# Performance work log

Measured on AMD Instinct MI355X. Metric: run time of the kernel, lower is better.

## Reference

```python
import jax, jax.numpy as jnp
import numpy as np

N_EMBD = 1024
EXPAND = 2
D_INNER = N_EMBD * EXPAND          # 2048
D_STATE = 64
N_HEADS = D_INNER // D_STATE       # 32
HEAD_DIM = D_INNER // N_HEADS      # 64
N_GROUPS = 1
D_CONV = 4
N_LAYERS = 48
BATCH, SEQ = 1, 512
PROJ_SIZE = 2 * D_INNER + N_HEADS + 2 * N_GROUPS * D_STATE  # 4256
EPS = 1e-6


def setup_inputs() -> dict:
    key = jax.random.key(0)
    ks = jax.random.split(key, 6)
    init_std = 0.02
    proj_std = 0.02 / np.sqrt(2 * N_LAYERS)
    return {
        "x": jax.random.normal(ks[0], (BATCH, SEQ, N_EMBD), jnp.float32),
        "norm_scale": jnp.ones((N_EMBD,), jnp.float32),
        "w_in": jax.random.normal(ks[1], (N_EMBD, PROJ_SIZE), jnp.float32) * init_std,
        "conv_weight": jax.random.normal(ks[2], (D_CONV, D_INNER), jnp.float32) * 0.02,
        "conv_bias": jnp.zeros((D_INNER,), jnp.float32),
        "A_log": jnp.log(0.5 + jnp.arange(N_HEADS, dtype=jnp.float32) * 0.5 / N_HEADS),
        "dt_bias": jax.random.normal(ks[3], (N_HEADS,), jnp.float32) * 0.1,
        "w_out": jax.random.normal(ks[4], (D_INNER, N_EMBD), jnp.float32) * proj_std,
    }


def _mamba_fwd(x, norm_scale, w_in, conv_weight, conv_bias, A_log, dt_bias, w_out):
    b, T, _ = x.shape
    residual = x
    # RMSNorm
    xn = x * jax.lax.rsqrt(jnp.mean(x * x, axis=-1, keepdims=True) + EPS) * norm_scale
    # in_proj and split
    proj = xn @ w_in  # (b, T, proj_size)
    gate = proj[..., :D_INNER]
    ssm_in = proj[..., D_INNER:2 * D_INNER]
    dt_raw = proj[..., 2 * D_INNER:2 * D_INNER + N_HEADS]
    gs = N_GROUPS * D_STATE
    B = proj[..., 2 * D_INNER + N_HEADS:2 * D_INNER + N_HEADS + gs].reshape(b, T, N_GROUPS, D_STATE)
    C = proj[..., 2 * D_INNER + N_HEADS + gs:].reshape(b, T, N_GROUPS, D_STATE)
    # causal depthwise short conv (cross-correlation, matching lax.conv semantics)
    xp = jnp.pad(ssm_in, ((0, 0), (D_CONV - 1, 0), (0, 0)))
    conv = conv_bias + sum(conv_weight[k] * xp[:, k:k + T, :] for k in range(D_CONV))
    h = jax.nn.silu(conv)  # (b, T, d_inner)
    dt = jax.nn.softplus(dt_raw + dt_bias)  # (b, T, H)
    A = -jnp.exp(A_log)  # (H,)
    A_bar = jnp.exp(A[None, None, :] * dt)  # (b, T, H)
    # heads / groups
    hpg = N_HEADS // N_GROUPS
    xh = h.reshape(b, T, N_HEADS, HEAD_DIM)
    Bh = jnp.repeat(B, hpg, axis=2)  # (b, T, H, N)
    Ch = jnp.repeat(C, hpg, axis=2)  # (b, T, H, N)
    # Bu[b,t,h,p,n] = B[b,t,h,n] * dt[b,t,h] * x[b,t,h,p]
    Bu = Bh[:, :, :, None, :] * (dt[..., None, None] * xh[..., None])  # (b,T,H,P,N)

    def _binary_op(left, right):
        a_l, b_l = left
        a_r, b_r = right
        return (a_l * a_r, a_r * b_l + b_r)

    # A_bar broadcast to (b,T,H,1,1) so the pair broadcasts against Bu
    _, states = jax.lax.associative_scan(_binary_op, (A_bar[..., None, None], Bu), axis=1)
    y = jnp.einsum('bthpn,bthn->bthp', states, Ch).reshape(b, T, D_INNER)
    y = y * jax.nn.silu(gate)
    y = y @ w_out
    return residual + y


def reference(x, norm_scale, w_in, conv_weight, conv_bias, A_log, dt_bias, w_out):
    return _mamba_fwd(x, norm_scale, w_in, conv_weight, conv_bias, A_log, dt_bias, w_out)
```

## Files before the change

kernel.cpp:

```cpp
#include <hip/hip_runtime.h>
#include <hip/hip_bf16.h>

typedef unsigned short u16;
typedef float f32x4v __attribute__((ext_vector_type(4)));
typedef short short8 __attribute__((ext_vector_type(8)));

#define TSEQ 512
#define EMB  1024
#define DI   2048
#define NH   32
#define DS   64
#define PROJ 4256
#define PROJP 4352
#define NCH  8
#define LCH  64
#define KSPLIT2 4

__device__ __forceinline__ u16 f2bf(float f) {
    union { __hip_bfloat16 h; u16 u; } cv;
    cv.h = __float2bfloat16(f);
    return cv.u;
}
__device__ __forceinline__ unsigned pack2(float a, float b) {
    return (unsigned)f2bf(a) | ((unsigned)f2bf(b) << 16);
}
__device__ __forceinline__ float silu(float v) { return v / (1.f + expf(-v)); }

__device__ __forceinline__ void transpose_tile(
        const float* __restrict__ src, u16* __restrict__ dst,
        int K, int N, int n0, int k0, int tid, float tile[64][68]) {
    const int lr = tid >> 4;
    const int lc = tid & 15;
    #pragma unroll
    for (int ps = 0; ps < 4; ++ps) {
        int r = ps * 16 + lr;
        float4 v;
        if (n0 + lc * 4 + 3 < N) {
            v = *(const float4*)&src[(size_t)(k0 + r) * N + n0 + lc * 4];
        } else {
            float t0 = 0.f, t1 = 0.f, t2 = 0.f, t3 = 0.f;
            int nb = n0 + lc * 4;
            if (nb + 0 < N) t0 = src[(size_t)(k0 + r) * N + nb + 0];
            if (nb + 1 < N) t1 = src[(size_t)(k0 + r) * N + nb + 1];
            if (nb + 2 < N) t2 = src[(size_t)(k0 + r) * N + nb + 2];
            if (nb + 3 < N) t3 = src[(size_t)(k0 + r) * N + nb + 3];
            v = make_float4(t0, t1, t2, t3);
        }
        *(float4*)&tile[r][lc * 4] = v;
    }
    __syncthreads();
    const int kk2 = (tid & 31) * 2;
    const int nr  = tid >> 5;
    #pragma unroll
    for (int ps = 0; ps < 8; ++ps) {
        int n = ps * 8 + nr;
        unsigned o = (unsigned)f2bf(tile[kk2][n]) | ((unsigned)f2bf(tile[kk2 + 1][n]) << 16);
        *(unsigned*)&dst[(size_t)(n0 + n) * K + k0 + kk2] = o;
    }
}

__global__ __launch_bounds__(256) void k_prep(
        const float* __restrict__ w_in, u16* __restrict__ w_inT,
        const float* __restrict__ w_out, u16* __restrict__ w_outT,
        const float* __restrict__ x, const float* __restrict__ scale,
        u16* __restrict__ xnb) {
    __shared__ float tile[64][68];
    const int b = blockIdx.x;
    const int tid = threadIdx.x;
    if (b < 1088) {
        int bx = b % 68, by = b / 68;
        transpose_tile(w_in, w_inT, 1024, PROJ, bx * 64, by * 64, tid, tile);
    } else if (b < 1600) {
        int b2 = b - 1088;
        int bx = b2 % 16, by = b2 / 16;
        transpose_tile(w_out, w_outT, 2048, 1024, bx * 64, by * 64, tid, tile);
    } else {
        int t = b - 1600;
        const float4* xr = (const float4*)(x + (size_t)t * EMB);
        float4 v = xr[tid];
        float ss = v.x * v.x + v.y * v.y + v.z * v.z + v.w * v.w;
        #pragma unroll
        for (int off = 32; off; off >>= 1) ss += __shfl_xor(ss, off);
        if ((tid & 63) == 0) tile[0][tid >> 6] = ss;
        __syncthreads();
        float tot = tile[0][0] + tile[0][1] + tile[0][2] + tile[0][3];
        float inv = rsqrtf(tot * (1.f / EMB) + 1e-6f);
        float4 s = ((const float4*)scale)[tid];
        uint2 o;
        o.x = pack2(v.x * inv * s.x, v.y * inv * s.y);
        o.y = pack2(v.z * inv * s.z, v.w * inv * s.w);
        ((uint2*)xnb)[(size_t)t * 256 + tid] = o;
    }
}

template<int BM, int BN>
__global__ __launch_bounds__(256) void k_gemm(
        const u16* __restrict__ A, int lda,
        const u16* __restrict__ BT, int ldb,
        float* __restrict__ C, int ldc, int Kper) {
    constexpr int WM = BM / 2, WN = BN / 2, FM = WM / 16, FN = WN / 16;
    constexpr int NA = BM * 8 / 256, NB = BN * 8 / 256;
    __shared__ __align__(16) u16 Al[BM][72];
    __shared__ __align__(16) u16 Bl[BN][72];
    const int tid = threadIdx.x;
    const int wid = tid >> 6, lane = tid & 63;
    const int wr = wid >> 1, wc = wid & 1;
    const int ar = lane & 15, kg = lane >> 4;
    const int row0 = blockIdx.y * BM, col0 = blockIdx.x * BN;
    const int kbase = blockIdx.z * Kper;
    const int Mtot = gridDim.y * BM;
    float* Cz = C + (size_t)blockIdx.z * Mtot * ldc;

    short8 ra[NA], rb[NB];
    auto load_stage = [&](int k0) {
        #pragma unroll
        for (int j = 0; j < NA; ++j) {
            int idx = tid + j * 256;
            ra[j] = *(const short8*)(A + (size_t)(row0 + (idx >> 3)) * lda + k0 + (idx & 7) * 8);
        }
        #pragma unroll
        for (int j = 0; j < NB; ++j) {
            int idx = tid + j * 256;
            rb[j] = *(const short8*)(BT + (size_t)(col0 + (idx >> 3)) * ldb + k0 + (idx & 7) * 8);
        }
    };
    auto write_stage = [&]() {
        #pragma unroll
        for (int j = 0; j < NA; ++j) {
            int idx = tid + j * 256;
            *(short8*)&Al[idx >> 3][(idx & 7) * 8] = ra[j];
        }
        #pragma unroll
        for (int j = 0; j < NB; ++j) {
            int idx = tid + j * 256;
            *(short8*)&Bl[idx >> 3][(idx & 7) * 8] = rb[j];
        }
    };

    f32x4v acc[FM][FN] = {};
    const int NT = Kper / 64;
    load_stage(kbase);
    for (int kt = 0; kt < NT; ++kt) {
        write_stage();
        __syncthreads();
        if (kt + 1 < NT) load_stage(kbase + (kt + 1) * 64);
        #pragma unroll
        for (int kk = 0; kk < 2; ++kk) {
            short8 af[FM], bf[FN];
            #pragma unroll
            for (int m = 0; m < FM; ++m)
                af[m] = *(const short8*)&Al[wr * WM + m * 16 + ar][kk * 32 + kg * 8];
            #pragma unroll
            for (int n = 0; n < FN; ++n)
                bf[n] = *(const short8*)&Bl[wc * WN + n * 16 + ar][kk * 32 + kg * 8];
            #pragma unroll
            for (int m = 0; m < FM; ++m)
                #pragma unroll
                for (int n = 0; n < FN; ++n)
                    acc[m][n] = __builtin_amdgcn_mfma_f32_16x16x32_bf16(
                        af[m], bf[n], acc[m][n], 0, 0, 0);
        }
        __syncthreads();
    }
    #pragma unroll
    for (int m = 0; m < FM; ++m)
        #pragma unroll
        for (int n = 0; n < FN; ++n)
            #pragma unroll
            for (int j = 0; j < 4; ++j) {
                int row = row0 + wr * WM + m * 16 + kg * 4 + j;
                int col = col0 + wc * WN + n * 16 + ar;
                Cz[(size_t)row * ldc + col] = acc[m][n][j];
            }
}

__global__ __launch_bounds__(256) void k_reduce_out(
        const float* __restrict__ part, const float* __restrict__ x,
        float* __restrict__ out) {
    int i = blockIdx.x * 256 + threadIdx.x;
    float4 v = ((const float4*)x)[i];
    #pragma unroll
    for (int z = 0; z < KSPLIT2; ++z) {
        float4 p = ((const float4*)part)[(size_t)z * (TSEQ * EMB / 4) + i];
        v.x += p.x; v.y += p.y; v.z += p.z; v.w += p.w;
    }
    ((float4*)out)[i] = v;
}

__global__ __launch_bounds__(256) void k_scan1f(
        const float* __restrict__ proj, const float* __restrict__ cw,
        const float* __restrict__ cb, const float* __restrict__ A_log,
        const float* __restrict__ dt_bias,
        float* __restrict__ Sloc, float* __restrict__ Pc) {
    const int c = blockIdx.x, h = blockIdx.y;
    const int tid = threadIdx.x;
    const int q = tid & 3, p = tid >> 2, n0 = q * 16;
    __shared__ __align__(16) float Blds[64][64];
    __shared__ __align__(16) float xt[67][64];
    __shared__ float al[64], dl[64];
    for (int i = tid; i < 4096; i += 256) {
        int t = i >> 6, n = i & 63;
        Blds[t][n] = proj[(size_t)(c * 64 + t) * PROJP + 2 * DI + NH + n];
    }
    for (int i = tid; i < 67 * 64; i += 256) {
        int r = i >> 6, n = i & 63;
        int tt = c * 64 - 3 + r;
        xt[r][n] = (tt >= 0) ? proj[(size_t)tt * PROJP + DI + h * 64 + n] : 0.f;
    }
    if (tid < 64) {
        float z = proj[(size_t)(c * 64 + tid) * PROJP + 2 * DI + h] + dt_bias[h];
        float dt = (z > 20.f) ? z : log1pf(expf(z));
        dl[tid] = dt;
        al[tid] = expf(-expf(A_log[h]) * dt);
    }
    __syncthreads();
    const int ch = h * 64 + p;
    const float cw0 = cw[0 * DI + ch], cw1 = cw[1 * DI + ch];
    const float cw2 = cw[2 * DI + ch], cw3 = cw[3 * DI + ch];
    const float cbv = cb[ch];
    float x0 = xt[0][p], x1 = xt[1][p], x2 = xt[2][p];
    float s[16] = {};
    for (int t = 0; t < 64; ++t) {
        float x3 = xt[t + 3][p];
        float cv = cbv + cw0 * x0 + cw1 * x1 + cw2 * x2 + cw3 * x3;
        x0 = x1; x1 = x2; x2 = x3;
        float hv = silu(cv);
        float a = al[t];
        float dtx = dl[t] * hv;
        const float4* brow = (const float4*)&Blds[t][n0];
        #pragma unroll
        for (int i4 = 0; i4 < 4; ++i4) {
            float4 b = brow[i4];
            s[i4*4+0] = a * s[i4*4+0] + dtx * b.x;
            s[i4*4+1] = a * s[i4*4+1] + dtx * b.y;
            s[i4*4+2] = a * s[i4*4+2] + dtx * b.z;
            s[i4*4+3] = a * s[i4*4+3] + dtx * b.w;
        }
    }
    float* dst = Sloc + ((size_t)(c * 32 + h) * 64 + p) * 64 + n0;
    #pragma unroll
    for (int i4 = 0; i4 < 4; ++i4)
        ((float4*)dst)[i4] = make_float4(s[i4*4], s[i4*4+1], s[i4*4+2], s[i4*4+3]);
    if (tid == 0) {
        float pr = 1.f;
        for (int t = 0; t < 64; ++t) pr *= al[t];
        Pc[c * 32 + h] = pr;
    }
}

__global__ __launch_bounds__(256) void k_scan3f(
        const float* __restrict__ proj, const float* __restrict__ cw,
        const float* __restrict__ cb, const float* __restrict__ A_log,
        const float* __restrict__ dt_bias,
        const float* __restrict__ Sloc, const float* __restrict__ Pc,
        u16* __restrict__ yg) {
    const int c = blockIdx.x, h = blockIdx.y;
    const int tid = threadIdx.x;
    const int q = tid & 3, p = tid >> 2, n0 = q * 16;
    __shared__ __align__(16) float Blds[64][64];
    __shared__ __align__(16) float Clds[64][64];
    __shared__ __align__(16) float xt[67][64];
    __shared__ float al[64], dl[64];
    for (int i = tid; i < 4096; i += 256) {
        int t = i >> 6, n = i & 63;
        Blds[t][n] = proj[(size_t)(c * 64 + t) * PROJP + 2 * DI + NH + n];
        Clds[t][n] = proj[(size_t)(c * 64 + t) * PROJP + 2 * DI + NH + DS + n];
    }
    for (int i = tid; i < 67 * 64; i += 256) {
        int r = i >> 6, n = i & 63;
        int tt = c * 64 - 3 + r;
        xt[r][n] = (tt >= 0) ? proj[(size_t)tt * PROJP + DI + h * 64 + n] : 0.f;
    }
    if (tid < 64) {
        float z = proj[(size_t)(c * 64 + tid) * PROJP + 2 * DI + h] + dt_bias[h];
        float dt = (z > 20.f) ? z : log1pf(expf(z));
        dl[tid] = dt;
        al[tid] = expf(-expf(A_log[h]) * dt);
    }
    __syncthreads();
    float s[16] = {};
    for (int j = 0; j < c; ++j) {
        float pcv = Pc[j * 32 + h];
        const float4* sj = (const float4*)(Sloc + ((size_t)(j * 32 + h) * 64 + p) * 64 + n0);
        #pragma unroll
        for (int i4 = 0; i4 < 4; ++i4) {
            float4 v = sj[i4];
            s[i4*4+0] = pcv * s[i4*4+0] + v.x;
            s[i4*4+1] = pcv * s[i4*4+1] + v.y;
            s[i4*4+2] = pcv * s[i4*4+2] + v.z;
            s[i4*4+3] = pcv * s[i4*4+3] + v.w;
        }
    }
    const int ch = h * 64 + p;
    const float cw0 = cw[0 * DI + ch], cw1 = cw[1 * DI + ch];
    const float cw2 = cw[2 * DI + ch], cw3 = cw[3 * DI + ch];
    const float cbv = cb[ch];
    float x0 = xt[0][p], x1 = xt[1][p], x2 = xt[2][p];
    for (int t = 0; t < 64; ++t) {
        float x3 = xt[t + 3][p];
        float cv = cbv + cw0 * x0 + cw1 * x1 + cw2 * x2 + cw3 * x3;
        x0 = x1; x1 = x2; x2 = x3;
        float hv = silu(cv);
        float a = al[t];
        float dtx = dl[t] * hv;
        const float4* brow = (const float4*)&Blds[t][n0];
        const float4* crow = (const float4*)&Clds[t][n0];
        float yp = 0.f;
        #pragma unroll
        for (int i4 = 0; i4 < 4; ++i4) {
            float4 b = brow[i4], cc = crow[i4];
            s[i4*4+0] = a * s[i4*4+0] + dtx * b.x; yp += s[i4*4+0] * cc.x;
            s[i4*4+1] = a * s[i4*4+1] + dtx * b.y; yp += s[i4*4+1] * cc.y;
            s[i4*4+2] = a * s[i4*4+2] + dtx * b.z; yp += s[i4*4+2] * cc.z;
            s[i4*4+3] = a * s[i4*4+3] + dtx * b.w; yp += s[i4*4+3] * cc.w;
        }
        yp += __shfl_xor(yp, 1);
        yp += __shfl_xor(yp, 2);
        if (q == 0) xt[t][p] = yp;
    }
    __syncthreads();
    for (int i = tid; i < 4096; i += 256) {
        int t = i >> 6, pp = i & 63;
        float y = xt[t][pp];
        float g = proj[(size_t)(c * 64 + t) * PROJP + h * 64 + pp];
        yg[(size_t)(c * 64 + t) * DI + h * 64 + pp] = f2bf(y * silu(g));
    }
}

extern "C" void kernel_launch(void* const* d_in, const int* in_sizes, int n_in,
                              void* d_out, int out_size, void* d_ws, size_t ws_size,
                              hipStream_t stream) {
    (void)in_sizes; (void)n_in; (void)out_size; (void)ws_size;
    const float* x       = (const float*)d_in[0];
    const float* nscale  = (const float*)d_in[1];
    const float* w_in    = (const float*)d_in[2];
    const float* conv_w  = (const float*)d_in[3];
    const float* conv_b  = (const float*)d_in[4];
    const float* A_log   = (const float*)d_in[5];
    const float* dt_bias = (const float*)d_in[6];
    const float* w_out   = (const float*)d_in[7];
    float* out = (float*)d_out;

    char* wsp = (char*)d_ws;
    auto alloc = [&](size_t bytes) {
        char* ptr = wsp;
        wsp += (bytes + 255) & ~(size_t)255;
        return ptr;
    };
    u16*   w_inT  = (u16*)  alloc((size_t)PROJP * 1024 * 2);
    u16*   w_outT = (u16*)  alloc((size_t)1024 * 2048 * 2);
    u16*   xnb    = (u16*)  alloc((size_t)512 * 1024 * 2);
    float* proj   = (float*)alloc((size_t)512 * PROJP * 4);
    float* Pc     = (float*)alloc((size_t)256 * 4);
    float* Sloc   = (float*)alloc((size_t)NCH * 32 * 4096 * 4);
    u16*   yg     = (u16*)  alloc((size_t)512 * 2048 * 2);
    float* part2  = (float*)alloc((size_t)KSPLIT2 * 512 * 1024 * 4);

    k_prep<<<2112, 256, 0, stream>>>(w_in, w_inT, w_out, w_outT, x, nscale, xnb);
    k_gemm<32, 128><<<dim3(34, 16, 1), 256, 0, stream>>>(
        xnb, 1024, w_inT, 1024, proj, PROJP, 1024);
    k_scan1f<<<dim3(NCH, 32), 256, 0, stream>>>(
        proj, conv_w, conv_b, A_log, dt_bias, Sloc, Pc);
    k_scan3f<<<dim3(NCH, 32), 256, 0, stream>>>(
        proj, conv_w, conv_b, A_log, dt_bias, Sloc, Pc, yg);
    k_gemm<32, 128><<<dim3(8, 16, KSPLIT2), 256, 0, stream>>>(
        yg, 2048, w_outT, 2048, part2, 1024, 2048 / KSPLIT2);
    k_reduce_out<<<512, 256, 0, stream>>>(part2, x, out);
}
```

Baseline: 171.6 us.

## Restructure chunked scan into local pass, inter-chunk state pass, and correction

The two-kernel chunked scan, which recomputed the local recurrence in the second pass, becomes three stages. First, a local intra-chunk scan emits per-chunk states, cumulative decay products and local outputs. Second, a small kernel propagates initial states across chunks. Third, a correction kernel adds the C·S_init·Pcum contribution and applies the gate. Chunk count doubles to 16 with 32 steps each, which raises parallelism and removes the serial recurrence recompute. The cost is extra global traffic for yloc and Sinit and one more launch.

```diff
diff --git a/kernel.cpp b/kernel.cpp
--- a/kernel.cpp
+++ b/kernel.cpp
@@ -12,8 +12,8 @@
 #define DS   64
 #define PROJ 4256
 #define PROJP 4352
-#define NCH  8
-#define LCH  64
+#define NCH  16
+#define LCH  32
 #define KSPLIT2 4
 
 __device__ __forceinline__ u16 f2bf(float f) {
@@ -187,116 +187,50 @@
     ((float4*)out)[i] = v;
 }
 
-__global__ __launch_bounds__(256) void k_scan1f(
+__global__ __launch_bounds__(256) void k_scan1g(
         const float* __restrict__ proj, const float* __restrict__ cw,
         const float* __restrict__ cb, const float* __restrict__ A_log,
         const float* __restrict__ dt_bias,
-        float* __restrict__ Sloc, float* __restrict__ Pc) {
+        float* __restrict__ Sloc, float* __restrict__ Pcum,
+        float* __restrict__ yloc) {
     const int c = blockIdx.x, h = blockIdx.y;
     const int tid = threadIdx.x;
     const int q = tid & 3, p = tid >> 2, n0 = q * 16;
-    __shared__ __align__(16) float Blds[64][64];
-    __shared__ __align__(16) float xt[67][64];
-    __shared__ float al[64], dl[64];
-    for (int i = tid; i < 4096; i += 256) {
+    __shared__ __align__(16) float Blds[LCH][64];
+    __shared__ __align__(16) float Clds[LCH][64];
+    __shared__ __align__(16) float xt[LCH + 3][64];
+    __shared__ float al[LCH], dl[LCH];
+    __shared__ float yl[LCH][64];
+    for (int i = tid; i < LCH * 64; i += 256) {
         int t = i >> 6, n = i & 63;
-        Blds[t][n] = proj[(size_t)(c * 64 + t) * PROJP + 2 * DI + NH + n];
-    }
-    for (int i = tid; i < 67 * 64; i += 256) {
+        Blds[t][n] = proj[(size_t)(c * LCH + t) * PROJP + 2 * DI + NH + n];
+        Clds[t][n] = proj[(size_t)(c * LCH + t) * PROJP + 2 * DI + NH + DS + n];
+    }
+    for (int i = tid; i < (LCH + 3) * 64; i += 256) {
         int r = i >> 6, n = i & 63;
-        int tt = c * 64 - 3 + r;
+        int tt = c * LCH - 3 + r;
         xt[r][n] = (tt >= 0) ? proj[(size_t)tt * PROJP + DI + h * 64 + n] : 0.f;
     }
-    if (tid < 64) {
-        float z = proj[(size_t)(c * 64 + tid) * PROJP + 2 * DI + h] + dt_bias[h];
+    if (tid < LCH) {
+        float z = proj[(size_t)(c * LCH + tid) * PROJP + 2 * DI + h] + dt_bias[h];
         float dt = (z > 20.f) ? z : log1pf(expf(z));
         dl[tid] = dt;
         al[tid] = expf(-expf(A_log[h]) * dt);
     }
     __syncthreads();
+    if (tid < LCH) {
+        float pr = 1.f;
+        #pragma unroll
+        for (int k = 0; k < LCH; ++k) if (k <= tid) pr *= al[k];
+        Pcum[((size_t)(c * 32 + h)) * LCH + tid] = pr;
+    }
     const int ch = h * 64 + p;
     const float cw0 = cw[0 * DI + ch], cw1 = cw[1 * DI + ch];
     const float cw2 = cw[2 * DI + ch], cw3 = cw[3 * DI + ch];
     const float cbv = cb[ch];
     float x0 = xt[0][p], x1 = xt[1][p], x2 = xt[2][p];
     float s[16] = {};
-    for (int t = 0; t < 64; ++t) {
-        float x3 = xt[t + 3][p];
-        float cv = cbv + cw0 * x0 + cw1 * x1 + cw2 * x2 + cw3 * x3;
-        x0 = x1; x1 = x2; x2 = x3;
-        float hv = silu(cv);
-        float a = al[t];
-        float dtx = dl[t] * hv;
-        const float4* brow = (const float4*)&Blds[t][n0];
-        #pragma unroll
-        for (int i4 = 0; i4 < 4; ++i4) {
-            float4 b = brow[i4];
-            s[i4*4+0] = a * s[i4*4+0] + dtx * b.x;
-            s[i4*4+1] = a * s[i4*4+1] + dtx * b.y;
-            s[i4*4+2] = a * s[i4*4+2] + dtx * b.z;
-            s[i4*4+3] = a * s[i4*4+3] + dtx * b.w;
-        }
-    }
-    float* dst = Sloc + ((size_t)(c * 32 + h) * 64 + p) * 64 + n0;
-    #pragma unroll
-    for (int i4 = 0; i4 < 4; ++i4)
-        ((float4*)dst)[i4] = make_float4(s[i4*4], s[i4*4+1], s[i4*4+2], s[i4*4+3]);
-    if (tid == 0) {
-        float pr = 1.f;
-        for (int t = 0; t < 64; ++t) pr *= al[t];
-        Pc[c * 32 + h] = pr;
-    }
-}
-
-__global__ __launch_bounds__(256) void k_scan3f(
-        const float* __restrict__ proj, const float* __restrict__ cw,
-        const float* __restrict__ cb, const float* __restrict__ A_log,
-        const float* __restrict__ dt_bias,
-        const float* __restrict__ Sloc, const float* __restrict__ Pc,
-        u16* __restrict__ yg) {
-    const int c = blockIdx.x, h = blockIdx.y;
-    const int tid = threadIdx.x;
-    const int q = tid & 3, p = tid >> 2, n0 = q * 16;
-    __shared__ __align__(16) float Blds[64][64];
-    __shared__ __align__(16) float Clds[64][64];
-    __shared__ __align__(16) float xt[67][64];
-    __shared__ float al[64], dl[64];
-    for (int i = tid; i < 4096; i += 256) {
-        int t = i >> 6, n = i & 63;
-        Blds[t][n] = proj[(size_t)(c * 64 + t) * PROJP + 2 * DI + NH + n];
-        Clds[t][n] = proj[(size_t)(c * 64 + t) * PROJP + 2 * DI + NH + DS + n];
-    }
-    for (int i = tid; i < 67 * 64; i += 256) {
-        int r = i >> 6, n = i & 63;
-        int tt = c * 64 - 3 + r;
-        xt[r][n] = (tt >= 0) ? proj[(size_t)tt * PROJP + DI + h * 64 + n] : 0.f;
-    }
-    if (tid < 64) {
-        float z = proj[(size_t)(c * 64 + tid) * PROJP + 2 * DI + h] + dt_bias[h];
-        float dt = (z > 20.f) ? z : log1pf(expf(z));
-        dl[tid] = dt;
-        al[tid] = expf(-expf(A_log[h]) * dt);
-    }
-    __syncthreads();
-    float s[16] = {};
-    for (int j = 0; j < c; ++j) {
-        float pcv = Pc[j * 32 + h];
-        const float4* sj = (const float4*)(Sloc + ((size_t)(j * 32 + h) * 64 + p) * 64 + n0);
-        #pragma unroll
-        for (int i4 = 0; i4 < 4; ++i4) {
-            float4 v = sj[i4];
-            s[i4*4+0] = pcv * s[i4*4+0] + v.x;
-            s[i4*4+1] = pcv * s[i4*4+1] + v.y;
-            s[i4*4+2] = pcv * s[i4*4+2] + v.z;
-            s[i4*4+3] = pcv * s[i4*4+3] + v.w;
-        }
-    }
-    const int ch = h * 64 + p;
-    const float cw0 = cw[0 * DI + ch], cw1 = cw[1 * DI + ch];
-    const float cw2 = cw[2 * DI + ch], cw3 = cw[3 * DI + ch];
-    const float cbv = cb[ch];
-    float x0 = xt[0][p], x1 = xt[1][p], x2 = xt[2][p];
-    for (int t = 0; t < 64; ++t) {
+    for (int t = 0; t < LCH; ++t) {
         float x3 = xt[t + 3][p];
         float cv = cbv + cw0 * x0 + cw1 * x1 + cw2 * x2 + cw3 * x3;
         x0 = x1; x1 = x2; x2 = x3;
@@ -316,14 +250,78 @@
         }
         yp += __shfl_xor(yp, 1);
         yp += __shfl_xor(yp, 2);
-        if (q == 0) xt[t][p] = yp;
-    }
-    __syncthreads();
+        if (q == 0) yl[t][p] = yp;
+    }
+    float* dst = Sloc + ((size_t)(c * 32 + h) * 64 + p) * 64 + n0;
+    #pragma unroll
+    for (int i4 = 0; i4 < 4; ++i4)
+        ((float4*)dst)[i4] = make_float4(s[i4*4], s[i4*4+1], s[i4*4+2], s[i4*4+3]);
+    __syncthreads();
+    for (int i = tid; i < LCH * 64; i += 256) {
+        int t = i >> 6, pp = i & 63;
+        yloc[(size_t)(c * LCH + t) * DI + h * 64 + pp] = yl[t][pp];
+    }
+}
+
+__global__ __launch_bounds__(256) void k_scan2(
+        const float* __restrict__ Sloc, const float* __restrict__ Pcum,
+        float* __restrict__ Sinit) {
+    int gid = blockIdx.x * 256 + threadIdx.x;
+    int h = gid >> 12, rem = gid & 4095;
+    float s = 0.f;
+    #pragma unroll
+    for (int cc = 0; cc < NCH; ++cc) {
+        size_t o = (size_t)(cc * 32 + h) * 4096 + rem;
+        Sinit[o] = s;
+        s = Pcum[((size_t)(cc * 32 + h)) * LCH + (LCH - 1)] * s + Sloc[o];
+    }
+}
+
+__global__ __launch_bounds__(256) void k_corr(
+        const float* __restrict__ proj, const float* __restrict__ Sinit,
+        const float* __restrict__ Pcum, const float* __restrict__ yloc,
+        u16* __restrict__ yg) {
+    const int c = blockIdx.x, h = blockIdx.y;
+    const int tid = threadIdx.x;
+    const int q = tid & 3, p = tid >> 2, n0 = q * 16;
+    __shared__ __align__(16) float Clds[LCH][64];
+    __shared__ __align__(16) float Sl[64][68];
+    __shared__ float Pl[LCH];
+    __shared__ float yl[LCH][64];
+    for (int i = tid; i < LCH * 64; i += 256) {
+        int t = i >> 6, n = i & 63;
+        Clds[t][n] = proj[(size_t)(c * LCH + t) * PROJP + 2 * DI + NH + DS + n];
+    }
     for (int i = tid; i < 4096; i += 256) {
+        Sl[i >> 6][i & 63] = Sinit[(size_t)(c * 32 + h) * 4096 + i];
+    }
+    if (tid < LCH) Pl[tid] = Pcum[((size_t)(c * 32 + h)) * LCH + tid];
+    __syncthreads();
+    float st[16];
+    #pragma unroll
+    for (int i4 = 0; i4 < 4; ++i4) {
+        float4 v = *(const float4*)&Sl[p][n0 + i4 * 4];
+        st[i4*4+0] = v.x; st[i4*4+1] = v.y; st[i4*4+2] = v.z; st[i4*4+3] = v.w;
+    }
+    for (int t = 0; t < LCH; ++t) {
+        const float4* crow = (const float4*)&Clds[t][n0];
+        float acc = 0.f;
+        #pragma unroll
+        for (int i4 = 0; i4 < 4; ++i4) {
+            float4 cc4 = crow[i4];
+            acc += st[i4*4+0] * cc4.x + st[i4*4+1] * cc4.y
+                 + st[i4*4+2] * cc4.z + st[i4*4+3] * cc4.w;
+        }
+        acc += __shfl_xor(acc, 1);
+        acc += __shfl_xor(acc, 2);
+        if (q == 0) yl[t][p] = acc * Pl[t];
+    }
+    __syncthreads();
+    for (int i = tid; i < LCH * 64; i += 256) {
         int t = i >> 6, pp = i & 63;
-        float y = xt[t][pp];
-        float g = proj[(size_t)(c * 64 + t) * PROJP + h * 64 + pp];
-        yg[(size_t)(c * 64 + t) * DI + h * 64 + pp] = f2bf(y * silu(g));
+        float y = yloc[(size_t)(c * LCH + t) * DI + h * 64 + pp] + yl[t][pp];
+        float g = proj[(size_t)(c * LCH + t) * PROJP + h * 64 + pp];
+        yg[(size_t)(c * LCH + t) * DI + h * 64 + pp] = f2bf(y * silu(g));
     }
 }
 
@@ -351,18 +349,20 @@
     u16*   w_outT = (u16*)  alloc((size_t)1024 * 2048 * 2);
     u16*   xnb    = (u16*)  alloc((size_t)512 * 1024 * 2);
     float* proj   = (float*)alloc((size_t)512 * PROJP * 4);
-    float* Pc     = (float*)alloc((size_t)256 * 4);
+    float* Pcum   = (float*)alloc((size_t)NCH * 32 * LCH * 4);
     float* Sloc   = (float*)alloc((size_t)NCH * 32 * 4096 * 4);
+    float* Sinit  = (float*)alloc((size_t)NCH * 32 * 4096 * 4);
+    float* yloc   = (float*)alloc((size_t)512 * 2048 * 4);
     u16*   yg     = (u16*)  alloc((size_t)512 * 2048 * 2);
     float* part2  = (float*)alloc((size_t)KSPLIT2 * 512 * 1024 * 4);
 
     k_prep<<<2112, 256, 0, stream>>>(w_in, w_inT, w_out, w_outT, x, nscale, xnb);
     k_gemm<32, 128><<<dim3(34, 16, 1), 256, 0, stream>>>(
         xnb, 1024, w_inT, 1024, proj, PROJP, 1024);
-    k_scan1f<<<dim3(NCH, 32), 256, 0, stream>>>(
-        proj, conv_w, conv_b, A_log, dt_bias, Sloc, Pc);
-    k_scan3f<<<dim3(NCH, 32), 256, 0, stream>>>(
-        proj, conv_w, conv_b, A_log, dt_bias, Sloc, Pc, yg);
+    k_scan1g<<<dim3(NCH, 32), 256, 0, stream>>>(
+        proj, conv_w, conv_b, A_log, dt_bias, Sloc, Pcum, yloc);
+    k_scan2<<<512, 256, 0, stream>>>(Sloc, Pcum, Sinit);
+    k_corr<<<dim3(NCH, 32), 256, 0, stream>>>(proj, Sinit, Pcum, yloc, yg);
     k_gemm<32, 128><<<dim3(8, 16, KSPLIT2), 256, 0, stream>>>(
         yg, 2048, w_outT, 2048, part2, 1024, 2048 / KSPLIT2);
     k_reduce_out<<<512, 256, 0, stream>>>(part2, x, out);
```

Result: faster. 155.4 us (-9.5%).
